# Kernel optimization log

Measured on AMD Instinct MI355X. Metric: run time of the kernel, lower is better.

## Reference

```python
import jax, jax.numpy as jnp
import numpy as np


def setup_inputs() -> dict:
    key = jax.random.key(0)
    k1, k2 = jax.random.split(key)
    B, T, D = 8, 2048, 2048
    layer_in = jax.random.normal(k1, (B, T, D), dtype=jnp.float32)
    # nn.Linear(2D, 2D): weight [out=2D, in=2D], bias [2D]
    W_gate = jax.random.normal(k2, (2 * D, 2 * D), dtype=jnp.float32) * 0.02
    b_gate = jnp.zeros((2 * D,), dtype=jnp.float32)
    return {"layer_in": layer_in, "W_gate": W_gate, "b_gate": b_gate}


def reference(layer_in, W_gate, b_gate):
    # Cumulative average: tril(ones)/row_index @ x  ==  cumsum(x)/[1..t]
    t = layer_in.shape[1]
    denom = jnp.arange(1, t + 1, dtype=layer_in.dtype)[:, None]  # (t, 1)
    average_out = jnp.cumsum(layer_in, axis=1) / denom  # (B, t, D)
    # Gating: Linear(2D -> 2D) on concat(x, avg), then chunk into two gates
    gating_in = jnp.concatenate([layer_in, average_out], axis=-1)  # (B, t, 2D)
    gates = jnp.einsum('btk,ok->bto', gating_in, W_gate) + b_gate  # (B, t, 2D)
    input_gate, forget_gate = jnp.split(gates, 2, axis=2)
    gating_out = (jax.nn.sigmoid(input_gate) * layer_in
                  + jax.nn.sigmoid(forget_gate) * average_out)
    return gating_out, average_out
```

## Files before the change

kernel.cpp:

```cpp
#include <hip/hip_runtime.h>
#include <hip/hip_bf16.h>


#define Bb 8
#define Tt 2048
#define Dd 2048
#define Mm (Bb * Tt)
#define Kk 4096
#define NC 32
#define CT 64

typedef __bf16 bf16x8 __attribute__((ext_vector_type(8)));
typedef float f32x4 __attribute__((ext_vector_type(4)));

__device__ __forceinline__ void gload16(const void* g, void* l) {
    __builtin_amdgcn_global_load_lds(
        (const __attribute__((address_space(1))) unsigned int*)g,
        (__attribute__((address_space(3))) unsigned int*)l, 16, 0, 0);
}

__global__ void wconv_kernel(const float* __restrict__ W,
                             unsigned short* __restrict__ Wb, long n) {
    long i = ((long)blockIdx.x * blockDim.x + threadIdx.x) * 4;
    long stride = (long)gridDim.x * blockDim.x * 4;
    for (; i < n; i += stride) {
        float4 v = *(const float4*)(W + i);
        __hip_bfloat16 a = __float2bfloat16(v.x);
        __hip_bfloat16 b = __float2bfloat16(v.y);
        __hip_bfloat16 c = __float2bfloat16(v.z);
        __hip_bfloat16 d = __float2bfloat16(v.w);
        ushort4 u;
        u.x = *(unsigned short*)&a; u.y = *(unsigned short*)&b;
        u.z = *(unsigned short*)&c; u.w = *(unsigned short*)&d;
        *(ushort4*)(Wb + i) = u;
    }
}

__global__ void ksum_kernel(const float* __restrict__ X, float* __restrict__ S) {
    int d = blockIdx.y * 256 + threadIdx.x;
    int bc = blockIdx.x;
    int b = bc >> 5, c = bc & 31;
    const float* p = X + ((long)(b * Tt + c * CT)) * Dd + d;
    float s = 0.f;
#pragma unroll 8
    for (int t = 0; t < CT; ++t) s += p[(long)t * Dd];
    S[(long)bc * Dd + d] = s;
}

__global__ void kscan_kernel(const float* __restrict__ X, const float* __restrict__ S,
                             float* __restrict__ AVG, unsigned short* __restrict__ Gin) {
    int d = blockIdx.y * 256 + threadIdx.x;
    int bc = blockIdx.x;
    int b = bc >> 5, c = bc & 31;
    const float* Sp = S + (long)(b * NC) * Dd + d;
    float run = 0.f;
    for (int cc = 0; cc < c; ++cc) run += Sp[(long)cc * Dd];
    const float* p = X + ((long)(b * Tt + c * CT)) * Dd + d;
    long row = (long)b * Tt + c * CT;
    for (int tt = 0; tt < CT; ++tt) {
        float x = p[(long)tt * Dd];
        run += x;
        float av = run / (float)(c * CT + tt + 1);
        long r = row + tt;
        AVG[r * Dd + d] = av;
        __hip_bfloat16 xb = __float2bfloat16(x);
        __hip_bfloat16 ab = __float2bfloat16(av);
        Gin[r * 4096 + d] = *(unsigned short*)&xb;
        Gin[r * 4096 + 2048 + d] = *(unsigned short*)&ab;
    }
}

#define MFMA(va, vb, c_) c_ = __builtin_amdgcn_mfma_f32_16x16x32_bf16(va, vb, c_, 0, 0, 0)
#define RD(p_, i_) (*(const bf16x8*)((p_) + (i_) * 1024))
#define SBAR __builtin_amdgcn_s_barrier()
#define SCHB __builtin_amdgcn_sched_barrier(0)

#define TILEBODY(t_, STG_)                                                      \
  {                                                                             \
    const int buf_ = (t_) & 3;                                                  \
    const char* pa_ = rA0 + buf_ * 32768;                                       \
    const char* pb_ = rB0 + buf_ * 32768;                                       \
              \
    bf16x8 a0 = RD(pa_,0), a1 = RD(pa_,1), a2 = RD(pa_,2), a3 = RD(pa_,3);      \
    bf16x8 b0 = RD(pb_,0), b1 = RD(pb_,1), b2 = RD(pb_,2), b3 = RD(pb_,3);      \
    if (STG_) { char* nd_ = ldsb + (((t_) + 3) & 3) * 32768 + woff;             \
      const long ko_ = ((long)(t_) + 3) * 64;                                   \
      gload16(gA0 + ko_, nd_); gload16(gA1 + ko_, nd_ + 8192); }                \
    SCHB; SBAR;                                                                 \
    asm volatile("s_waitcnt lgkmcnt(0)" ::: "memory"); SCHB;                    \
    __builtin_amdgcn_s_setprio(1);                                              \
    MFMA(a0,b0,acc[0][0]); MFMA(a0,b1,acc[0][1]); MFMA(a0,b2,acc[0][2]); MFMA(a0,b3,acc[0][3]); \
    MFMA(a1,b0,acc[1][0]); MFMA(a1,b1,acc[1][1]); MFMA(a1,b2,acc[1][2]); MFMA(a1,b3,acc[1][3]); \
    MFMA(a2,b0,acc[2][0]); MFMA(a2,b1,acc[2][1]); MFMA(a2,b2,acc[2][2]); MFMA(a2,b3,acc[2][3]); \
    MFMA(a3,b0,acc[3][0]); MFMA(a3,b1,acc[3][1]); MFMA(a3,b2,acc[3][2]); MFMA(a3,b3,acc[3][3]); \
    __builtin_amdgcn_s_setprio(0); SCHB; SBAR;                                  \
                   \
    bf16x8 a4 = RD(pa_,4), a5 = RD(pa_,5), a6 = RD(pa_,6), a7 = RD(pa_,7);      \
    if (STG_) { char* nd_ = ldsb + (((t_) + 3) & 3) * 32768 + 16384 + woff;     \
      const long ko_ = ((long)(t_) + 3) * 64;                                   \
      gload16(gB0 + ko_, nd_); gload16(gB1 + ko_, nd_ + 8192); }                \
    SCHB; SBAR;                                                                 \
    asm volatile("s_waitcnt lgkmcnt(0)" ::: "memory"); SCHB;                    \
    __builtin_amdgcn_s_setprio(1);                                              \
    MFMA(a4,b0,acc[4][0]); MFMA(a4,b1,acc[4][1]); MFMA(a4,b2,acc[4][2]); MFMA(a4,b3,acc[4][3]); \
    MFMA(a5,b0,acc[5][0]); MFMA(a5,b1,acc[5][1]); MFMA(a5,b2,acc[5][2]); MFMA(a5,b3,acc[5][3]); \
    MFMA(a6,b0,acc[6][0]); MFMA(a6,b1,acc[6][1]); MFMA(a6,b2,acc[6][2]); MFMA(a6,b3,acc[6][3]); \
    MFMA(a7,b0,acc[7][0]); MFMA(a7,b1,acc[7][1]); MFMA(a7,b2,acc[7][2]); MFMA(a7,b3,acc[7][3]); \
    __builtin_amdgcn_s_setprio(0); SCHB;                                        \
  }

#define BOUNDARY(N_)                                                            \
  asm volatile("s_waitcnt vmcnt(" #N_ ")" ::: "memory");                        \
  SBAR; SCHB;

__global__ __launch_bounds__(512, 1) void gemm2p_kernel(
    const unsigned short* __restrict__ Gin,
    const unsigned short* __restrict__ Wb,
    const float* __restrict__ bias,
    float* __restrict__ OUT)
{
    __shared__ __attribute__((aligned(128))) char lds[131072];
    char* ldsb = (char*)lds;

    const int tid = threadIdx.x;
    const int w = tid >> 6, l = tid & 63;
    const int wm = w >> 2, wn = w & 3;
    const int lm = l & 15;
    const int woff = w * 1024;

    const int bid = blockIdx.x;
    const int batch = bid >> 8;
    const int rr = bid & 255;
    const int xcd = rr & 7;
    const int j = rr >> 3;
    const int nt = xcd * 2 + (j >> 4);
    const int mt = batch * 16 + (j & 15);
    const long m0 = (long)mt * 256;
    const int n0 = nt * 128;

    const int srow = tid >> 2;
    const int schunk = (tid & 3) ^ ((tid >> 3) & 3);
    const char* gA0 = (const char*)Gin + (m0 + srow) * 8192 + schunk * 16;
    const char* gA1 = gA0 + 128 * 8192;
    const long jr0 = n0 + ((srow >> 6) << 5) + (srow & 31) + (((srow >> 5) & 1) << 11);
    const int j1 = 128 + srow;
    const long jr1 = n0 + ((j1 >> 6) << 5) + (j1 & 31) + (((j1 >> 5) & 1) << 11);
    const char* gB0 = (const char*)Wb + jr0 * 8192 + schunk * 16;
    const char* gB1 = (const char*)Wb + jr1 * 8192 + schunk * 16;

    const int cbyte = (((l >> 4) ^ ((lm >> 1) & 3))) * 16;
    const char* rA0 = ldsb + (wm * 128 + lm) * 64 + cbyte;
    const char* rB0 = ldsb + 16384 + (wn * 64 + lm) * 64 + cbyte;

    f32x4 acc[8][4] = {};

    {
        gload16(gA0,       ldsb + woff);
        gload16(gA1,       ldsb + 8192 + woff);
        gload16(gB0,       ldsb + 16384 + woff);
        gload16(gB1,       ldsb + 24576 + woff);
        gload16(gA0 + 64,  ldsb + 32768 + woff);
        gload16(gA1 + 64,  ldsb + 32768 + 8192 + woff);
        gload16(gB0 + 64,  ldsb + 32768 + 16384 + woff);
        gload16(gB1 + 64,  ldsb + 32768 + 24576 + woff);
        gload16(gA0 + 128, ldsb + 65536 + woff);
        gload16(gA1 + 128, ldsb + 65536 + 8192 + woff);
        gload16(gB0 + 128, ldsb + 65536 + 16384 + woff);
        gload16(gB1 + 128, ldsb + 65536 + 24576 + woff);
    }
    BOUNDARY(8);

#pragma unroll 1
    for (int t = 0; t < 125; ++t) {
        TILEBODY(t, 1);
        BOUNDARY(8);
    }
    TILEBODY(125, 0);
    BOUNDARY(4);
    TILEBODY(126, 0);
    BOUNDARY(0);
    TILEBODY(127, 0);

#pragma unroll
    for (int mi = 0; mi < 8; ++mi) {
        long rbase = m0 + wm * 128 + mi * 16 + (l >> 4) * 4;
#pragma unroll
        for (int nj = 0; nj < 2; ++nj) {
            int d = n0 + wn * 32 + nj * 16 + lm;
            float bi_ = bias[d];
            float bf_ = bias[d + 2048];
#pragma unroll
            for (int r = 0; r < 4; ++r) {
                long row = rbase + r;
                unsigned int ux = Gin[row * 4096 + d];
                unsigned int ua = Gin[row * 4096 + 2048 + d];
                union { unsigned int u; float f; } cx, ca;
                cx.u = ux << 16; ca.u = ua << 16;
                float gi = acc[mi][nj][r] + bi_;
                float gf = acc[mi][nj + 2][r] + bf_;
                float si = 1.f / (1.f + __expf(-gi));
                float sf = 1.f / (1.f + __expf(-gf));
                OUT[row * 2048 + d] = si * cx.f + sf * ca.f;
            }
        }
    }
}

extern "C" void kernel_launch(void* const* d_in, const int* in_sizes, int n_in,
                              void* d_out, int out_size, void* d_ws, size_t ws_size,
                              hipStream_t stream) {
    const float* X = (const float*)d_in[0];
    const float* W = (const float*)d_in[1];
    const float* bias = (const float*)d_in[2];

    float* OUT = (float*)d_out;
    float* AVG = OUT + (long)Mm * Dd;

    char* ws = (char*)d_ws;
    unsigned short* Wb  = (unsigned short*)ws;
    unsigned short* Gin = (unsigned short*)(ws + 33554432);
    float* S = (float*)(ws + 33554432 + 134217728);

    wconv_kernel<<<2048, 256, 0, stream>>>(W, Wb, (long)Kk * Kk);
    ksum_kernel<<<dim3(Bb * NC, Dd / 256), 256, 0, stream>>>(X, S);
    kscan_kernel<<<dim3(Bb * NC, Dd / 256), 256, 0, stream>>>(X, S, AVG, Gin);
    gemm2p_kernel<<<1024, 512, 0, stream>>>(Gin, Wb, bias, OUT);
}
```

Baseline: 634.7 us.

## Restructure GEMM pipeline into double-buffered 64KB stages of two K-subtiles

```diff
diff --git a/kernel.cpp b/kernel.cpp
--- a/kernel.cpp
+++ b/kernel.cpp
@@ -74,46 +74,62 @@
 #define RD(p_, i_) (*(const bf16x8*)((p_) + (i_) * 1024))
 #define SBAR __builtin_amdgcn_s_barrier()
 #define SCHB __builtin_amdgcn_sched_barrier(0)
-
-#define TILEBODY(t_, STG_)                                                      \
+#define LGKM0 asm volatile("s_waitcnt lgkmcnt(0)" ::: "memory")
+
+#define CL_LO(A0_, A1_, A2_, A3_, B0_, B1_, B2_, B3_)                           \
+    __builtin_amdgcn_s_setprio(1);                                              \
+    MFMA(A0_,B0_,acc[0][0]); MFMA(A0_,B1_,acc[0][1]); MFMA(A0_,B2_,acc[0][2]); MFMA(A0_,B3_,acc[0][3]); \
+    MFMA(A1_,B0_,acc[1][0]); MFMA(A1_,B1_,acc[1][1]); MFMA(A1_,B2_,acc[1][2]); MFMA(A1_,B3_,acc[1][3]); \
+    MFMA(A2_,B0_,acc[2][0]); MFMA(A2_,B1_,acc[2][1]); MFMA(A2_,B2_,acc[2][2]); MFMA(A2_,B3_,acc[2][3]); \
+    MFMA(A3_,B0_,acc[3][0]); MFMA(A3_,B1_,acc[3][1]); MFMA(A3_,B2_,acc[3][2]); MFMA(A3_,B3_,acc[3][3]); \
+    __builtin_amdgcn_s_setprio(0);
+#define CL_HI(A4_, A5_, A6_, A7_, B0_, B1_, B2_, B3_)                           \
+    __builtin_amdgcn_s_setprio(1);                                              \
+    MFMA(A4_,B0_,acc[4][0]); MFMA(A4_,B1_,acc[4][1]); MFMA(A4_,B2_,acc[4][2]); MFMA(A4_,B3_,acc[4][3]); \
+    MFMA(A5_,B0_,acc[5][0]); MFMA(A5_,B1_,acc[5][1]); MFMA(A5_,B2_,acc[5][2]); MFMA(A5_,B3_,acc[5][3]); \
+    MFMA(A6_,B0_,acc[6][0]); MFMA(A6_,B1_,acc[6][1]); MFMA(A6_,B2_,acc[6][2]); MFMA(A6_,B3_,acc[6][3]); \
+    MFMA(A7_,B0_,acc[7][0]); MFMA(A7_,B1_,acc[7][1]); MFMA(A7_,B2_,acc[7][2]); MFMA(A7_,B3_,acc[7][3]); \
+    __builtin_amdgcn_s_setprio(0);
+
+#define TILE64(t_, bb_, STG_, V1_, V3_)                                         \
   {                                                                             \
-    const int buf_ = (t_) & 3;                                                  \
-    const char* pa_ = rA0 + buf_ * 32768;                                       \
-    const char* pb_ = rB0 + buf_ * 32768;                                       \
-              \
+    const char* pa_ = rA0 + (bb_);                                              \
+    const char* pb_ = rB0 + (bb_);                                              \
+    char* nb_ = ldsb + ((bb_) ^ 65536) + woff;                                  \
+    const long ko_ = ((long)(t_) + 1) * 128;                                    \
+          \
     bf16x8 a0 = RD(pa_,0), a1 = RD(pa_,1), a2 = RD(pa_,2), a3 = RD(pa_,3);      \
     bf16x8 b0 = RD(pb_,0), b1 = RD(pb_,1), b2 = RD(pb_,2), b3 = RD(pb_,3);      \
-    if (STG_) { char* nd_ = ldsb + (((t_) + 3) & 3) * 32768 + woff;             \
-      const long ko_ = ((long)(t_) + 3) * 64;                                   \
-      gload16(gA0 + ko_, nd_); gload16(gA1 + ko_, nd_ + 8192); }                \
+    if (STG_) { gload16(gA0 + ko_, nb_); gload16(gA1 + ko_, nb_ + 8192); }      \
+    SCHB; SBAR; LGKM0; SCHB;                                                    \
+    CL_LO(a0, a1, a2, a3, b0, b1, b2, b3)                                       \
     SCHB; SBAR;                                                                 \
-    asm volatile("s_waitcnt lgkmcnt(0)" ::: "memory"); SCHB;                    \
-    __builtin_amdgcn_s_setprio(1);                                              \
-    MFMA(a0,b0,acc[0][0]); MFMA(a0,b1,acc[0][1]); MFMA(a0,b2,acc[0][2]); MFMA(a0,b3,acc[0][3]); \
-    MFMA(a1,b0,acc[1][0]); MFMA(a1,b1,acc[1][1]); MFMA(a1,b2,acc[1][2]); MFMA(a1,b3,acc[1][3]); \
-    MFMA(a2,b0,acc[2][0]); MFMA(a2,b1,acc[2][1]); MFMA(a2,b2,acc[2][2]); MFMA(a2,b3,acc[2][3]); \
-    MFMA(a3,b0,acc[3][0]); MFMA(a3,b1,acc[3][1]); MFMA(a3,b2,acc[3][2]); MFMA(a3,b3,acc[3][3]); \
-    __builtin_amdgcn_s_setprio(0); SCHB; SBAR;                                  \
-                   \
+       \
     bf16x8 a4 = RD(pa_,4), a5 = RD(pa_,5), a6 = RD(pa_,6), a7 = RD(pa_,7);      \
-    if (STG_) { char* nd_ = ldsb + (((t_) + 3) & 3) * 32768 + 16384 + woff;     \
-      const long ko_ = ((long)(t_) + 3) * 64;                                   \
-      gload16(gB0 + ko_, nd_); gload16(gB1 + ko_, nd_ + 8192); }                \
+    if (STG_) { gload16(gB0 + ko_, nb_ + 16384); gload16(gB1 + ko_, nb_ + 24576); } \
+    SCHB; SBAR; LGKM0; SCHB;                                                    \
+    CL_HI(a4, a5, a6, a7, b0, b1, b2, b3)                                       \
+    SCHB;                                                                       \
+    asm volatile("s_waitcnt vmcnt(" #V1_ ")" ::: "memory");                     \
+    SBAR;                                                                       \
+          \
+    bf16x8 c0 = RD(pa_+32768,0), c1 = RD(pa_+32768,1), c2 = RD(pa_+32768,2), c3 = RD(pa_+32768,3); \
+    bf16x8 d0 = RD(pb_+32768,0), d1 = RD(pb_+32768,1), d2 = RD(pb_+32768,2), d3 = RD(pb_+32768,3); \
+    if (STG_) { gload16(gA0 + ko_ + 64, nb_ + 32768); gload16(gA1 + ko_ + 64, nb_ + 40960); } \
+    SCHB; SBAR; LGKM0; SCHB;                                                    \
+    CL_LO(c0, c1, c2, c3, d0, d1, d2, d3)                                       \
     SCHB; SBAR;                                                                 \
-    asm volatile("s_waitcnt lgkmcnt(0)" ::: "memory"); SCHB;                    \
-    __builtin_amdgcn_s_setprio(1);                                              \
-    MFMA(a4,b0,acc[4][0]); MFMA(a4,b1,acc[4][1]); MFMA(a4,b2,acc[4][2]); MFMA(a4,b3,acc[4][3]); \
-    MFMA(a5,b0,acc[5][0]); MFMA(a5,b1,acc[5][1]); MFMA(a5,b2,acc[5][2]); MFMA(a5,b3,acc[5][3]); \
-    MFMA(a6,b0,acc[6][0]); MFMA(a6,b1,acc[6][1]); MFMA(a6,b2,acc[6][2]); MFMA(a6,b3,acc[6][3]); \
-    MFMA(a7,b0,acc[7][0]); MFMA(a7,b1,acc[7][1]); MFMA(a7,b2,acc[7][2]); MFMA(a7,b3,acc[7][3]); \
-    __builtin_amdgcn_s_setprio(0); SCHB;                                        \
+       \
+    bf16x8 c4 = RD(pa_+32768,4), c5 = RD(pa_+32768,5), c6 = RD(pa_+32768,6), c7 = RD(pa_+32768,7); \
+    if (STG_) { gload16(gB0 + ko_ + 64, nb_ + 49152); gload16(gB1 + ko_ + 64, nb_ + 57344); } \
+    SCHB; SBAR; LGKM0; SCHB;                                                    \
+    CL_HI(c4, c5, c6, c7, d0, d1, d2, d3)                                       \
+    SCHB;                                                                       \
+    asm volatile("s_waitcnt vmcnt(" #V3_ ")" ::: "memory");                     \
+    SBAR;                                                                       \
   }
 
-#define BOUNDARY(N_)                                                            \
-  asm volatile("s_waitcnt vmcnt(" #N_ ")" ::: "memory");                        \
-  SBAR; SCHB;
-
-__global__ __launch_bounds__(512, 1) void gemm2p_kernel(
+__global__ __launch_bounds__(512, 1) void gemm64_kernel(
     const unsigned short* __restrict__ Gin,
     const unsigned short* __restrict__ Wb,
     const float* __restrict__ bias,
@@ -154,32 +170,24 @@
 
     f32x4 acc[8][4] = {};
 
-    {
-        gload16(gA0,       ldsb + woff);
-        gload16(gA1,       ldsb + 8192 + woff);
-        gload16(gB0,       ldsb + 16384 + woff);
-        gload16(gB1,       ldsb + 24576 + woff);
-        gload16(gA0 + 64,  ldsb + 32768 + woff);
-        gload16(gA1 + 64,  ldsb + 32768 + 8192 + woff);
-        gload16(gB0 + 64,  ldsb + 32768 + 16384 + woff);
-        gload16(gB1 + 64,  ldsb + 32768 + 24576 + woff);
-        gload16(gA0 + 128, ldsb + 65536 + woff);
-        gload16(gA1 + 128, ldsb + 65536 + 8192 + woff);
-        gload16(gB0 + 128, ldsb + 65536 + 16384 + woff);
-        gload16(gB1 + 128, ldsb + 65536 + 24576 + woff);
-    }
-    BOUNDARY(8);
+    gload16(gA0,      ldsb + woff);
+    gload16(gA1,      ldsb + 8192 + woff);
+    gload16(gB0,      ldsb + 16384 + woff);
+    gload16(gB1,      ldsb + 24576 + woff);
+    gload16(gA0 + 64, ldsb + 32768 + woff);
+    gload16(gA1 + 64, ldsb + 40960 + woff);
+    gload16(gB0 + 64, ldsb + 49152 + woff);
+    gload16(gB1 + 64, ldsb + 57344 + woff);
+    asm volatile("s_waitcnt vmcnt(4)" ::: "memory");
+    SBAR; SCHB;
 
 #pragma unroll 1
-    for (int t = 0; t < 125; ++t) {
-        TILEBODY(t, 1);
-        BOUNDARY(8);
-    }
-    TILEBODY(125, 0);
-    BOUNDARY(4);
-    TILEBODY(126, 0);
-    BOUNDARY(0);
-    TILEBODY(127, 0);
+    for (int t = 0; t < 62; t += 2) {
+        TILE64(t,     0,     1, 4, 4)
+        TILE64(t + 1, 65536, 1, 4, 4)
+    }
+    TILE64(62, 0,     1, 4, 4)
+    TILE64(63, 65536, 0, 0, 0)
 
 #pragma unroll
     for (int mi = 0; mi < 8; ++mi) {
@@ -224,5 +232,5 @@
     wconv_kernel<<<2048, 256, 0, stream>>>(W, Wb, (long)Kk * Kk);
     ksum_kernel<<<dim3(Bb * NC, Dd / 256), 256, 0, stream>>>(X, S);
     kscan_kernel<<<dim3(Bb * NC, Dd / 256), 256, 0, stream>>>(X, S, AVG, Gin);
-    gemm2p_kernel<<<1024, 512, 0, stream>>>(Gin, Wb, bias, OUT);
-}
+    gemm64_kernel<<<1024, 512, 0, stream>>>(Gin, Wb, bias, OUT);
+}
```

Result: faster. 615.6 us (-3.0%).

## Switch GEMM to double-buffered LDS with two blocks per CU

Applied to the files above, without the earlier changes.

```diff
diff --git a/kernel.cpp b/kernel.cpp
--- a/kernel.cpp
+++ b/kernel.cpp
@@ -75,17 +75,16 @@
 #define SBAR __builtin_amdgcn_s_barrier()
 #define SCHB __builtin_amdgcn_sched_barrier(0)
 
-#define TILEBODY(t_, STG_)                                                      \
+#define TILEBODY(t_, bb_, STG_)                                                 \
   {                                                                             \
-    const int buf_ = (t_) & 3;                                                  \
-    const char* pa_ = rA0 + buf_ * 32768;                                       \
-    const char* pb_ = rB0 + buf_ * 32768;                                       \
+    const char* pa_ = rA0 + (bb_);                                              \
+    const char* pb_ = rB0 + (bb_);                                              \
+    char* nb_ = ldsb + ((bb_) ^ 32768) + woff;                                  \
+    const long ko_ = ((long)(t_) + 1) * 64;                                     \
               \
     bf16x8 a0 = RD(pa_,0), a1 = RD(pa_,1), a2 = RD(pa_,2), a3 = RD(pa_,3);      \
     bf16x8 b0 = RD(pb_,0), b1 = RD(pb_,1), b2 = RD(pb_,2), b3 = RD(pb_,3);      \
-    if (STG_) { char* nd_ = ldsb + (((t_) + 3) & 3) * 32768 + woff;             \
-      const long ko_ = ((long)(t_) + 3) * 64;                                   \
-      gload16(gA0 + ko_, nd_); gload16(gA1 + ko_, nd_ + 8192); }                \
+    if (STG_) { gload16(gA0 + ko_, nb_); gload16(gA1 + ko_, nb_ + 8192); }      \
     SCHB; SBAR;                                                                 \
     asm volatile("s_waitcnt lgkmcnt(0)" ::: "memory"); SCHB;                    \
     __builtin_amdgcn_s_setprio(1);                                              \
@@ -94,11 +93,9 @@
     MFMA(a2,b0,acc[2][0]); MFMA(a2,b1,acc[2][1]); MFMA(a2,b2,acc[2][2]); MFMA(a2,b3,acc[2][3]); \
     MFMA(a3,b0,acc[3][0]); MFMA(a3,b1,acc[3][1]); MFMA(a3,b2,acc[3][2]); MFMA(a3,b3,acc[3][3]); \
     __builtin_amdgcn_s_setprio(0); SCHB; SBAR;                                  \
-                   \
+         \
     bf16x8 a4 = RD(pa_,4), a5 = RD(pa_,5), a6 = RD(pa_,6), a7 = RD(pa_,7);      \
-    if (STG_) { char* nd_ = ldsb + (((t_) + 3) & 3) * 32768 + 16384 + woff;     \
-      const long ko_ = ((long)(t_) + 3) * 64;                                   \
-      gload16(gB0 + ko_, nd_); gload16(gB1 + ko_, nd_ + 8192); }                \
+    if (STG_) { gload16(gB0 + ko_, nb_ + 16384); gload16(gB1 + ko_, nb_ + 24576); } \
     SCHB; SBAR;                                                                 \
     asm volatile("s_waitcnt lgkmcnt(0)" ::: "memory"); SCHB;                    \
     __builtin_amdgcn_s_setprio(1);                                              \
@@ -107,19 +104,17 @@
     MFMA(a6,b0,acc[6][0]); MFMA(a6,b1,acc[6][1]); MFMA(a6,b2,acc[6][2]); MFMA(a6,b3,acc[6][3]); \
     MFMA(a7,b0,acc[7][0]); MFMA(a7,b1,acc[7][1]); MFMA(a7,b2,acc[7][2]); MFMA(a7,b3,acc[7][3]); \
     __builtin_amdgcn_s_setprio(0); SCHB;                                        \
+    asm volatile("s_waitcnt vmcnt(0)" ::: "memory");                            \
+    SBAR; SCHB;                                                                 \
   }
 
-#define BOUNDARY(N_)                                                            \
-  asm volatile("s_waitcnt vmcnt(" #N_ ")" ::: "memory");                        \
-  SBAR; SCHB;
-
-__global__ __launch_bounds__(512, 1) void gemm2p_kernel(
+__global__ __launch_bounds__(512, 2) void gemm2b_kernel(
     const unsigned short* __restrict__ Gin,
     const unsigned short* __restrict__ Wb,
     const float* __restrict__ bias,
     float* __restrict__ OUT)
 {
-    __shared__ __attribute__((aligned(128))) char lds[131072];
+    __shared__ __attribute__((aligned(128))) char lds[65536];
     char* ldsb = (char*)lds;
 
     const int tid = threadIdx.x;
@@ -154,32 +149,20 @@
 
     f32x4 acc[8][4] = {};
 
-    {
-        gload16(gA0,       ldsb + woff);
-        gload16(gA1,       ldsb + 8192 + woff);
-        gload16(gB0,       ldsb + 16384 + woff);
-        gload16(gB1,       ldsb + 24576 + woff);
-        gload16(gA0 + 64,  ldsb + 32768 + woff);
-        gload16(gA1 + 64,  ldsb + 32768 + 8192 + woff);
-        gload16(gB0 + 64,  ldsb + 32768 + 16384 + woff);
-        gload16(gB1 + 64,  ldsb + 32768 + 24576 + woff);
-        gload16(gA0 + 128, ldsb + 65536 + woff);
-        gload16(gA1 + 128, ldsb + 65536 + 8192 + woff);
-        gload16(gB0 + 128, ldsb + 65536 + 16384 + woff);
-        gload16(gB1 + 128, ldsb + 65536 + 24576 + woff);
-    }
-    BOUNDARY(8);
+    gload16(gA0, ldsb + woff);
+    gload16(gA1, ldsb + 8192 + woff);
+    gload16(gB0, ldsb + 16384 + woff);
+    gload16(gB1, ldsb + 24576 + woff);
+    asm volatile("s_waitcnt vmcnt(0)" ::: "memory");
+    SBAR; SCHB;
 
 #pragma unroll 1
-    for (int t = 0; t < 125; ++t) {
-        TILEBODY(t, 1);
-        BOUNDARY(8);
-    }
-    TILEBODY(125, 0);
-    BOUNDARY(4);
-    TILEBODY(126, 0);
-    BOUNDARY(0);
-    TILEBODY(127, 0);
+    for (int t = 0; t < 126; t += 2) {
+        TILEBODY(t,     0,     1)
+        TILEBODY(t + 1, 32768, 1)
+    }
+    TILEBODY(126, 0,     1)
+    TILEBODY(127, 32768, 0)
 
 #pragma unroll
     for (int mi = 0; mi < 8; ++mi) {
@@ -224,5 +207,5 @@
     wconv_kernel<<<2048, 256, 0, stream>>>(W, Wb, (long)Kk * Kk);
     ksum_kernel<<<dim3(Bb * NC, Dd / 256), 256, 0, stream>>>(X, S);
     kscan_kernel<<<dim3(Bb * NC, Dd / 256), 256, 0, stream>>>(X, S, AVG, Gin);
-    gemm2p_kernel<<<1024, 512, 0, stream>>>(Gin, Wb, bias, OUT);
-}
+    gemm2b_kernel<<<1024, 512, 0, stream>>>(Gin, Wb, bias, OUT);
+}
```

Result: slower. 707.3 us (+11.4%).
